# Kernel tuning notes

Hardware: AMD Instinct MI355X
Metric: run time of the kernel (lower is better)

## Reference

```python
import jax, jax.numpy as jnp
import numpy as np

BN_EPS = 1e-5

def conv1x1(x, w, b):
    # x: [B,C,H,W], w: [O,C], b: [O]
    return jnp.einsum('bchw,oc->bohw', x, w) + b[None, :, None, None]

def maxpool2x2(x):
    B, C, H, W = x.shape
    return x.reshape(B, C, H // 2, 2, W // 2, 2).max(axis=(3, 5))

def setup_inputs() -> dict:
    key = jax.random.key(0)
    ks = jax.random.split(key, 11)
    B, C, H, W = 8, 256, 64, 64
    Ci = C // 2  # inter_channels = 128
    s_in = 1.0 / np.sqrt(C)
    s_int = 1.0 / np.sqrt(Ci)
    return {
        'x': jax.random.normal(ks[0], (B, C, H, W), jnp.float32),
        'theta_w': jax.random.uniform(ks[1], (Ci, C), jnp.float32, -s_in, s_in),
        'theta_b': jax.random.uniform(ks[2], (Ci,), jnp.float32, -s_in, s_in),
        'phi_w': jax.random.uniform(ks[3], (Ci, C), jnp.float32, -s_in, s_in),
        'phi_b': jax.random.uniform(ks[4], (Ci,), jnp.float32, -s_in, s_in),
        'g_w': jax.random.uniform(ks[5], (Ci, C), jnp.float32, -s_in, s_in),
        'g_b': jax.random.uniform(ks[6], (Ci,), jnp.float32, -s_in, s_in),
        'W_w': jax.random.uniform(ks[7], (C, Ci), jnp.float32, -s_int, s_int),
        'W_b': jax.random.uniform(ks[8], (C,), jnp.float32, -s_int, s_int),
        'bn_gamma': jax.random.normal(ks[9], (C,), jnp.float32) * 0.1 + 1.0,
        'bn_beta': jax.random.normal(ks[10], (C,), jnp.float32) * 0.1,
    }

def reference(x, theta_w, theta_b, phi_w, phi_b, g_w, g_b, W_w, W_b, bn_gamma, bn_beta):
    B, C, H, W = x.shape
    Ci = theta_w.shape[0]
    # g and phi are sub-sampled (2x2 maxpool) after the 1x1 conv
    g_x = maxpool2x2(conv1x1(x, g_w, g_b)).reshape(B, Ci, -1)        # [B,Ci,M]
    g_x = g_x.transpose(0, 2, 1)                                     # [B,M,Ci]
    theta_x = conv1x1(x, theta_w, theta_b).reshape(B, Ci, -1)        # [B,Ci,N]
    theta_x = theta_x.transpose(0, 2, 1)                             # [B,N,Ci]
    phi_x = maxpool2x2(conv1x1(x, phi_w, phi_b)).reshape(B, Ci, -1)  # [B,Ci,M]
    f = jnp.einsum('bnc,bcm->bnm', theta_x, phi_x)                   # [B,N,M]
    f_div_C = jax.nn.softmax(f, axis=-1)
    y = jnp.einsum('bnm,bmc->bnc', f_div_C, g_x)                     # [B,N,Ci]
    y = y.transpose(0, 2, 1).reshape(B, Ci, H, W)
    # 1x1 conv + BatchNorm2d (training-mode batch statistics)
    W_y = conv1x1(y, W_w, W_b)
    mean = W_y.mean(axis=(0, 2, 3))
    var = W_y.var(axis=(0, 2, 3))
    W_y = (W_y - mean[None, :, None, None]) * jax.lax.rsqrt(var + BN_EPS)[None, :, None, None]
    W_y = W_y * bn_gamma[None, :, None, None] + bn_beta[None, :, None, None]
    return W_y + x
```

## Files before the change

### kernel.cpp

```cpp
#include <hip/hip_runtime.h>
#include <hip/hip_bf16.h>
#include <cstdint>
#include <math.h>

using bf16 = __hip_bfloat16;
typedef __attribute__((ext_vector_type(8))) short bf16x8;
typedef __attribute__((ext_vector_type(4))) float f32x4;

#define DEV __device__ __forceinline__

DEV float b2f(unsigned short u) { return __uint_as_float(((uint32_t)u) << 16); }
DEV float bfl(bf16 h) { return __bfloat162float(h); }
DEV short f2bs(float f) { bf16 h = __float2bfloat16(f); return *(short*)&h; }
DEV uint32_t pk2(float a, float b) {
  return (uint32_t)(unsigned short)f2bs(a) |
         ((uint32_t)(unsigned short)f2bs(b) << 16);
}
DEV float ldv(const void* p, int isbf, int i) {
  return isbf ? bfl(((const bf16*)p)[i]) : ((const float*)p)[i];
}

DEV bf16x8 load_wfrag(const void* w, int isbf, int row, int K, int off) {
  bf16x8 r;
  if (isbf) {
    r = *(const bf16x8*)((const short*)w + (size_t)row * K + off);
  } else {
    const float* f = (const float*)w + (size_t)row * K + off;
    float4 a = *(const float4*)f, b = *(const float4*)(f + 4);
    r[0] = f2bs(a.x); r[1] = f2bs(a.y); r[2] = f2bs(a.z); r[3] = f2bs(a.w);
    r[4] = f2bs(b.x); r[5] = f2bs(b.y); r[6] = f2bs(b.z); r[7] = f2bs(b.w);
  }
  return r;
}

__global__ __launch_bounds__(256) void sniff_kernel(
    const unsigned short* __restrict__ xr, int* __restrict__ flag)
{
  int tid = threadIdx.x;
  int good = 0;
  for (int k = tid; k < 16384; k += 256) {
    unsigned short u = xr[2 * k];
    int e = (u >> 7) & 0xFF;
    good += (e >= 0x6A && e <= 0x86) ? 1 : 0;
  }
  __shared__ int r[256];
  r[tid] = good;
  __syncthreads();
  for (int off = 128; off; off >>= 1) {
    if (tid < off) r[tid] += r[tid + off];
    __syncthreads();
  }
  if (tid == 0) *flag = (r[0] > 9830) ? 1 : 0;
}

__global__ __launch_bounds__(256) void transpose_x(
    const void* __restrict__ x, short* __restrict__ xT, const int* __restrict__ flag)
{
  const int isbf = *flag;
  __shared__ short lt[64 * 71];
  const int n0 = blockIdx.x * 64, c0 = blockIdx.y * 64, b = blockIdx.z;
  const int tid = threadIdx.x;
  for (int it = 0; it < 4; ++it) {
    int idx4 = it * 256 + tid;
    int ci = idx4 >> 4, n4 = (idx4 & 15) * 4;
    size_t go = ((size_t)(b * 256 + c0 + ci)) * 4096 + n0 + n4;
    if (isbf) {
      ushort4 v = *(const ushort4*)((const unsigned short*)x + go);
      lt[ci * 71 + n4 + 0] = v.x; lt[ci * 71 + n4 + 1] = v.y;
      lt[ci * 71 + n4 + 2] = v.z; lt[ci * 71 + n4 + 3] = v.w;
    } else {
      float4 v = *(const float4*)((const float*)x + go);
      lt[ci * 71 + n4 + 0] = f2bs(v.x); lt[ci * 71 + n4 + 1] = f2bs(v.y);
      lt[ci * 71 + n4 + 2] = f2bs(v.z); lt[ci * 71 + n4 + 3] = f2bs(v.w);
    }
  }
  __syncthreads();
  for (int it = 0; it < 4; ++it) {
    int idx4 = it * 256 + tid;
    int n = idx4 >> 4, c4 = (idx4 & 15) * 4;
    ushort4 v;
    v.x = (unsigned short)lt[(c4 + 0) * 71 + n];
    v.y = (unsigned short)lt[(c4 + 1) * 71 + n];
    v.z = (unsigned short)lt[(c4 + 2) * 71 + n];
    v.w = (unsigned short)lt[(c4 + 3) * 71 + n];
    *(ushort4*)(xT + ((size_t)(b * 4096 + n0 + n)) * 256 + c0 + c4) = v;
  }
}

__global__ __launch_bounds__(256) void conv_t_k(
    const short* __restrict__ xT, const void* __restrict__ w,
    const void* __restrict__ bias, short* __restrict__ out,
    const int* __restrict__ flag)
{
  const int isbf = *flag;
  __shared__ short sh[64 * 264];
  const int b = blockIdx.y, nbase = blockIdx.x * 64, tid = threadIdx.x;
  const int ln = tid & 15, q = (tid >> 4) & 3, wv = tid >> 6;
  for (int it = 0; it < 16; ++it) {
    int idx4 = it * 256 + tid;
    int n = idx4 >> 6, c4 = (idx4 & 63) * 4;
    *(ushort4*)&sh[n * 264 + c4] =
        *(const ushort4*)(xT + ((size_t)(b * 4096 + nbase + n)) * 256 + c4);
  }
  __syncthreads();
  f32x4 zero = {0.f, 0.f, 0.f, 0.f};
  f32x4 acc[4][2];
  for (int nt = 0; nt < 4; ++nt) for (int ti = 0; ti < 2; ++ti) acc[nt][ti] = zero;

  for (int kk = 0; kk < 8; ++kk) {
    int off = kk * 32 + q * 8;
    bf16x8 a[4];
    #pragma unroll
    for (int nt = 0; nt < 4; ++nt)
      a[nt] = *(const bf16x8*)&sh[(16 * nt + ln) * 264 + off];
    #pragma unroll
    for (int ti = 0; ti < 2; ++ti) {
      bf16x8 bw = load_wfrag(w, isbf, 16 * (2 * wv + ti) + ln, 256, off);
      #pragma unroll
      for (int nt = 0; nt < 4; ++nt)
        acc[nt][ti] = __builtin_amdgcn_mfma_f32_16x16x32_bf16(a[nt], bw, acc[nt][ti], 0, 0, 0);
    }
  }
  __syncthreads();
  float bv[2];
  for (int ti = 0; ti < 2; ++ti) bv[ti] = ldv(bias, isbf, 16 * (2 * wv + ti) + ln);
  for (int nt = 0; nt < 4; ++nt)
    for (int ti = 0; ti < 2; ++ti)
      for (int r = 0; r < 4; ++r)
        sh[(16 * nt + q * 4 + r) * 136 + 16 * (2 * wv + ti) + ln] =
            f2bs(acc[nt][ti][r] + bv[ti]);
  __syncthreads();
  for (int it = 0; it < 8; ++it) {
    int idx4 = it * 256 + tid;
    int n = idx4 >> 5, c4 = (idx4 & 31) * 4;
    *(ushort4*)(out + ((size_t)(b * 4096 + nbase + n)) * 128 + c4) =
        *(const ushort4*)&sh[n * 136 + c4];
  }
}

template<int CO, int K>
__global__ __launch_bounds__(256) void conv_n_k(
    const short* __restrict__ inp, const void* __restrict__ w,
    const void* __restrict__ bias, short* __restrict__ out,
    const int* __restrict__ flag)
{
  const int isbf = *flag;
  constexpr int XS = 64 * (K + 8);
  constexpr int OS = CO * 68;
  __shared__ short sh[(XS > OS ? XS : OS)];
  const int b = blockIdx.y, nbase = blockIdx.x * 64, tid = threadIdx.x;
  const int ln = tid & 15, q = (tid >> 4) & 3, wv = tid >> 6;
  constexpr int TPW = CO / 64;
  constexpr int KS = (K == 256) ? 6 : 5;
  for (int it = 0; it < 64 * K / 1024; ++it) {
    int idx4 = it * 256 + tid;
    int n = idx4 >> KS, c4 = (idx4 & ((K / 4) - 1)) * 4;
    *(ushort4*)&sh[n * (K + 8) + c4] =
        *(const ushort4*)(inp + ((size_t)(b * 4096 + nbase + n)) * K + c4);
  }
  __syncthreads();
  f32x4 zero = {0.f, 0.f, 0.f, 0.f};
  f32x4 acc[TPW][4];
  for (int ti = 0; ti < TPW; ++ti) for (int nt = 0; nt < 4; ++nt) acc[ti][nt] = zero;

  for (int kk = 0; kk < K / 32; ++kk) {
    int off = kk * 32 + q * 8;
    bf16x8 bx[4];
    #pragma unroll
    for (int nt = 0; nt < 4; ++nt)
      bx[nt] = *(const bf16x8*)&sh[(16 * nt + ln) * (K + 8) + off];
    #pragma unroll
    for (int ti = 0; ti < TPW; ++ti) {
      bf16x8 aw = load_wfrag(w, isbf, 16 * (TPW * wv + ti) + ln, K, off);
      #pragma unroll
      for (int nt = 0; nt < 4; ++nt)
        acc[ti][nt] = __builtin_amdgcn_mfma_f32_16x16x32_bf16(aw, bx[nt], acc[ti][nt], 0, 0, 0);
    }
  }
  __syncthreads();
  for (int ti = 0; ti < TPW; ++ti)
    for (int r = 0; r < 4; ++r) {
      int co = 16 * (TPW * wv + ti) + q * 4 + r;
      float bb = ldv(bias, isbf, co);
      for (int nt = 0; nt < 4; ++nt)
        sh[co * 68 + 16 * nt + ln] = f2bs(acc[ti][nt][r] + bb);
    }
  __syncthreads();
  for (int it = 0; it < 64 * CO / 1024; ++it) {
    int idx4 = it * 256 + tid;
    int co = idx4 >> 4, n4 = (idx4 & 15) * 4;
    *(ushort4*)(out + ((size_t)(b * CO + co)) * 4096 + nbase + n4) =
        *(const ushort4*)&sh[co * 68 + n4];
  }
}

__global__ __launch_bounds__(256) void pool_phi_kernel(
    const short* __restrict__ pc, short* __restrict__ phi)
{
  int idx = blockIdx.x * 256 + threadIdx.x;
  int ci = idx & 127, m = (idx >> 7) & 1023, b = idx >> 17;
  int mh = m >> 5, mw = m & 31;
  const short* p = pc + ((size_t)(b * 4096 + (mh * 2) * 64 + mw * 2)) * 128 + ci;
  float v = fmaxf(fmaxf(b2f(p[0]), b2f(p[128])),
                  fmaxf(b2f(p[64 * 128]), b2f(p[65 * 128])));
  phi[idx] = f2bs(v);
}

__global__ __launch_bounds__(256) void pool_g_kernel(
    const short* __restrict__ gc, short* __restrict__ g)
{
  int idx = blockIdx.x * 256 + threadIdx.x;
  int m = idx & 1023, bc = idx >> 10;
  int mh = m >> 5, mw = m & 31;
  const short* p = gc + (size_t)bc * 4096 + mh * 128 + mw * 2;
  float v = fmaxf(fmaxf(b2f(p[0]), b2f(p[1])), fmaxf(b2f(p[64]), b2f(p[65])));
  g[idx] = f2bs(v);
}

__global__ __launch_bounds__(256) void attn_kernel(
    const short* __restrict__ theta, const short* __restrict__ phi,
    const short* __restrict__ g, short* __restrict__ y)
{
  __shared__ short ph[64 * 136];
  __shared__ short gl[128 * 72];
  __shared__ short Pl[64 * 72];
  const int b = blockIdx.y, nbase = blockIdx.x * 64, tid = threadIdx.x;
  const int ln = tid & 15, q = (tid >> 4) & 3, wv = tid >> 6;

  const int pm  = tid >> 5;
  const int pc4 = (tid & 31) * 4;
  const int gci = tid >> 4;
  const int gm4 = (tid & 15) * 4;
  const short* phb = phi + (size_t)b * 1024 * 128;
  const short* gb  = g   + (size_t)b * 128 * 1024;

  ushort4 pf_p[8], pf_g[8];
  #pragma unroll
  for (int it = 0; it < 8; ++it)
    pf_p[it] = *(const ushort4*)(phb + ((size_t)(pm + 8 * it)) * 128 + pc4);
  #pragma unroll
  for (int it = 0; it < 8; ++it)
    pf_g[it] = *(const ushort4*)(gb + ((size_t)(gci + 16 * it)) * 1024 + gm4);

  bf16x8 a[4];
  #pragma unroll
  for (int kk = 0; kk < 4; ++kk)
    a[kk] = *(const bf16x8*)(theta +
        ((size_t)(b * 4096 + nbase + 16 * wv + ln)) * 128 + kk * 32 + q * 8);

  f32x4 zero = {0.f, 0.f, 0.f, 0.f};
  f32x4 yacc[8], lacc = zero;
  #pragma unroll
  for (int t = 0; t < 8; ++t) yacc[t] = zero;
  bf16x8 ones;
  #pragma unroll
  for (int j = 0; j < 8; ++j) ones[j] = 0x3F80;

  for (int mc = 0; mc < 16; ++mc) {
    #pragma unroll
    for (int it = 0; it < 8; ++it)
      *(ushort4*)&ph[(pm + 8 * it) * 136 + pc4] = pf_p[it];
    #pragma unroll
    for (int it = 0; it < 8; ++it)
      *(ushort4*)&gl[(gci + 16 * it) * 72 + gm4] = pf_g[it];
    __syncthreads();

    if (mc < 15) {
      const int nmc = mc + 1;
      #pragma unroll
      for (int it = 0; it < 8; ++it)
        pf_p[it] = *(const ushort4*)(phb +
            ((size_t)(nmc * 64 + pm + 8 * it)) * 128 + pc4);
      #pragma unroll
      for (int it = 0; it < 8; ++it)
        pf_g[it] = *(const ushort4*)(gb +
            ((size_t)(gci + 16 * it)) * 1024 + nmc * 64 + gm4);
    }

    #pragma unroll
    for (int t = 0; t < 4; ++t) {
      f32x4 s = zero;
      #pragma unroll
      for (int kk = 0; kk < 4; ++kk) {
        bf16x8 bp = *(const bf16x8*)&ph[(16 * t + ln) * 136 + kk * 32 + q * 8];
        s = __builtin_amdgcn_mfma_f32_16x16x32_bf16(a[kk], bp, s, 0, 0, 0);
      }
      #pragma unroll
      for (int r = 0; r < 4; ++r)
        Pl[(16 * wv + q * 4 + r) * 72 + 16 * t + ln] =
            f2bs(__expf(fminf(s[r], 80.f)));
    }
    bf16x8 ap[2];
    #pragma unroll
    for (int kk = 0; kk < 2; ++kk)
      ap[kk] = *(const bf16x8*)&Pl[(16 * wv + ln) * 72 + kk * 32 + q * 8];
    #pragma unroll
    for (int kk = 0; kk < 2; ++kk)
      lacc = __builtin_amdgcn_mfma_f32_16x16x32_bf16(ap[kk], ones, lacc, 0, 0, 0);
    #pragma unroll
    for (int t = 0; t < 8; ++t) {
      #pragma unroll
      for (int kk = 0; kk < 2; ++kk) {
        bf16x8 bg = *(const bf16x8*)&gl[(16 * t + ln) * 72 + kk * 32 + q * 8];
        yacc[t] = __builtin_amdgcn_mfma_f32_16x16x32_bf16(ap[kk], bg, yacc[t], 0, 0, 0);
      }
    }
    __syncthreads();
  }

  float li[4];
  #pragma unroll
  for (int r = 0; r < 4; ++r) li[r] = 1.0f / lacc[r];
  for (int t = 0; t < 8; ++t)
    for (int r = 0; r < 4; ++r)
      ph[(16 * wv + q * 4 + r) * 136 + 16 * t + ln] = f2bs(yacc[t][r] * li[r]);
  __syncthreads();
  for (int it = 0; it < 8; ++it) {
    int idx4 = it * 256 + tid;
    int n = idx4 >> 5, c4 = (idx4 & 31) * 4;
    *(ushort4*)(y + ((size_t)(b * 4096 + nbase + n)) * 128 + c4) =
        *(const ushort4*)&ph[n * 136 + c4];
  }
}

__global__ __launch_bounds__(256, 4) void convW_k(
    const short* __restrict__ yb, const void* __restrict__ w,
    const void* __restrict__ bias, short* __restrict__ Wy,
    float* __restrict__ stats, const int* __restrict__ flag)
{
  const int isbf = *flag;
  __shared__ short sh[256 * 72];
  const int b = blockIdx.y, nbase = blockIdx.x * 64, tid = threadIdx.x;
  const int ln = tid & 15, q = (tid >> 4) & 3, wv = tid >> 6;

  for (int it = 0; it < 4; ++it) {
    int idx8 = it * 256 + tid;
    int n = idx8 >> 4, c8 = (idx8 & 15) * 8;
    *(uint4*)&sh[n * 136 + c8] =
        *(const uint4*)(yb + ((size_t)(b * 4096 + nbase + n)) * 128 + c8);
  }
  __syncthreads();
  f32x4 zero = {0.f, 0.f, 0.f, 0.f};
  f32x4 acc[4][4];
  for (int ti = 0; ti < 4; ++ti)
    for (int nt = 0; nt < 4; ++nt) acc[ti][nt] = zero;

  for (int kk = 0; kk < 4; ++kk) {
    int off = kk * 32 + q * 8;
    bf16x8 bx[4];
    #pragma unroll
    for (int nt = 0; nt < 4; ++nt)
      bx[nt] = *(const bf16x8*)&sh[(16 * nt + ln) * 136 + off];
    #pragma unroll
    for (int ti = 0; ti < 4; ++ti) {
      bf16x8 aw = load_wfrag(w, isbf, 16 * (4 * wv + ti) + ln, 128, off);
      #pragma unroll
      for (int nt = 0; nt < 4; ++nt)
        acc[ti][nt] = __builtin_amdgcn_mfma_f32_16x16x32_bf16(aw, bx[nt], acc[ti][nt], 0, 0, 0);
    }
  }
  __syncthreads();
  #pragma unroll
  for (int ti = 0; ti < 4; ++ti)
    #pragma unroll
    for (int r = 0; r < 4; ++r) {
      int co = 16 * (4 * wv + ti) + 4 * q + r;
      float bb = ldv(bias, isbf, co);
      #pragma unroll
      for (int nt = 0; nt < 4; ++nt)
        sh[co * 72 + 16 * nt + ln] = f2bs(acc[ti][nt][r] + bb);
    }
  __syncthreads();
  {
    int co = tid;
    float s = 0.f, s2 = 0.f;
    for (int i = 0; i < 64; ++i) {
      float v = b2f((unsigned short)sh[co * 72 + i]);
      s += v; s2 += v * v;
    }
    atomicAdd(&stats[co], s);
    atomicAdd(&stats[256 + co], s2);
  }
  for (int it = 0; it < 8; ++it) {
    int idx8 = it * 256 + tid;
    int co = idx8 >> 3, n8 = (idx8 & 7) * 8;
    *(uint4*)(Wy + ((size_t)(b * 256 + co)) * 4096 + nbase + n8) =
        *(const uint4*)&sh[co * 72 + n8];
  }
}

__global__ __launch_bounds__(256) void bn_apply4(
    const short* __restrict__ Wy, const void* __restrict__ x,
    const float* __restrict__ stats, const void* __restrict__ gamma,
    const void* __restrict__ beta, void* __restrict__ out,
    const int* __restrict__ flag)
{
  const int isbf = *flag;
  int t = blockIdx.x * 256 + threadIdx.x;
  int idx4 = t * 4;
  int c = (idx4 >> 12) & 255;
  float s = stats[c], s2 = stats[256 + c];
  float mean = s * (1.0f / 32768.0f);
  float var = fmaxf(s2 * (1.0f / 32768.0f) - mean * mean, 0.f);
  float scale = rsqrtf(var + 1e-5f) * ldv(gamma, isbf, c);
  float shift = ldv(beta, isbf, c) - mean * scale;
  ushort4 wy = *(const ushort4*)(Wy + idx4);
  float xv[4];
  if (isbf) {
    ushort4 xu = *(const ushort4*)((const unsigned short*)x + idx4);
    xv[0] = b2f(xu.x); xv[1] = b2f(xu.y); xv[2] = b2f(xu.z); xv[3] = b2f(xu.w);
  } else {
    float4 xf = *(const float4*)((const float*)x + idx4);
    xv[0] = xf.x; xv[1] = xf.y; xv[2] = xf.z; xv[3] = xf.w;
  }
  float v0 = b2f(wy.x) * scale + shift + xv[0];
  float v1 = b2f(wy.y) * scale + shift + xv[1];
  float v2 = b2f(wy.z) * scale + shift + xv[2];
  float v3 = b2f(wy.w) * scale + shift + xv[3];
  if (isbf) {
    uint2 o; o.x = pk2(v0, v1); o.y = pk2(v2, v3);
    *(uint2*)((unsigned short*)out + idx4) = o;
  } else {
    float4 o = make_float4(v0, v1, v2, v3);
    *(float4*)((float*)out + idx4) = o;
  }
}

extern "C" void kernel_launch(void* const* d_in, const int* in_sizes, int n_in,
                              void* d_out, int out_size, void* d_ws, size_t ws_size,
                              hipStream_t stream) {
  const void* x       = d_in[0];
  const void* theta_w = d_in[1];
  const void* theta_b = d_in[2];
  const void* phi_w   = d_in[3];
  const void* phi_b   = d_in[4];
  const void* g_w     = d_in[5];
  const void* g_b     = d_in[6];
  const void* W_w     = d_in[7];
  const void* W_b     = d_in[8];
  const void* gamma   = d_in[9];
  const void* beta    = d_in[10];

  char* wsb = (char*)d_ws;
  short* xT      = (short*)(wsb + 0);
  short* ybuf    = (short*)(wsb + 0);
  short* theta   = (short*)(wsb + 16777216);
  short* W_y     = (short*)(wsb + 16777216);
  short* scratch = (short*)(wsb + 25165824);
  short* phi     = (short*)(wsb + 33554432);
  short* gg      = (short*)(wsb + 35651584);
  float* stats   = (float*)(wsb + 37748736);
  int*   flag    = (int*)  (wsb + 37750784);

  dim3 blk(256);
  dim3 cgrid(64, 8);
  dim3 tgrid(64, 4, 8);

  hipMemsetAsync(stats, 0, 2048, stream);
  sniff_kernel<<<1, blk, 0, stream>>>((const unsigned short*)x, flag);
  transpose_x<<<tgrid, blk, 0, stream>>>(x, xT, flag);
  conv_t_k<<<cgrid, blk, 0, stream>>>(xT, theta_w, theta_b, theta, flag);
  conv_t_k<<<cgrid, blk, 0, stream>>>(xT, phi_w, phi_b, scratch, flag);
  pool_phi_kernel<<<4096, blk, 0, stream>>>(scratch, phi);
  conv_n_k<128, 256><<<cgrid, blk, 0, stream>>>(xT, g_w, g_b, scratch, flag);
  pool_g_kernel<<<4096, blk, 0, stream>>>(scratch, gg);
  attn_kernel<<<cgrid, blk, 0, stream>>>(theta, phi, gg, ybuf);
  convW_k<<<cgrid, blk, 0, stream>>>(ybuf, W_w, W_b, W_y, stats, flag);
  bn_apply4<<<8192, blk, 0, stream>>>(W_y, x, stats, gamma, beta, d_out, flag);
}
```

Before: 246.7 us.

## Restructure attention kernel with 32x32 MFMA, register-resident P and split-M waves

The attention kernel now uses 32x32x16 bf16 MFMAs in a transposed formulation (phi as A, theta as B). The softmax probabilities are converted in registers with v_cvt_pk_bf16 and rearranged with v_permlane32_swap, so the LDS round trip for P goes away. Each wave handles a 32-row n-half and a 32-column m-half, and the partial y accumulators and row sums are combined through shared memory at the end. The shared-memory tiles use XOR swizzling with 16-byte loads, and the row-sum MFMA against a ones vector is replaced by scalar adds. The costs are more registers (launch bounds of 2), a cross-wave reduction epilogue, and reliance on gfx950-specific instructions.

Result: slower. 353.2 us (+43.2%).

```diff
diff --git a/kernel.cpp b/kernel.cpp
--- a/kernel.cpp
+++ b/kernel.cpp
@@ -6,6 +6,7 @@
 using bf16 = __hip_bfloat16;
 typedef __attribute__((ext_vector_type(8))) short bf16x8;
 typedef __attribute__((ext_vector_type(4))) float f32x4;
+typedef __attribute__((ext_vector_type(16))) float f32x16;
 
 #define DEV __device__ __forceinline__
 
@@ -18,6 +19,11 @@
 }
 DEV float ldv(const void* p, int isbf, int i) {
   return isbf ? bfl(((const bf16*)p)[i]) : ((const float*)p)[i];
+}
+DEV uint32_t cvtpk_bf16(float a, float b) {
+  uint32_t r;
+  asm("v_cvt_pk_bf16_f32 %0, %1, %2" : "=v"(r) : "v"(a), "v"(b));
+  return r;
 }
 
 DEV bf16x8 load_wfrag(const void* w, int isbf, int row, int K, int off) {
@@ -217,109 +223,152 @@
   g[idx] = f2bs(v);
 }
 
-__global__ __launch_bounds__(256) void attn_kernel(
+__global__ __launch_bounds__(256, 2) void attn_kernel(
     const short* __restrict__ theta, const short* __restrict__ phi,
     const short* __restrict__ g, short* __restrict__ y)
 {
-  __shared__ short ph[64 * 136];
-  __shared__ short gl[128 * 72];
-  __shared__ short Pl[64 * 72];
+  __shared__ alignas(16) char smem[51712];
+  char* phs = smem;
+  char* gls = smem + 16384;
+  float* comb = (float*)smem;
+  float* lred = (float*)(smem + 33792);
+  short* yout = (short*)(smem + 34304);
+
   const int b = blockIdx.y, nbase = blockIdx.x * 64, tid = threadIdx.x;
-  const int ln = tid & 15, q = (tid >> 4) & 3, wv = tid >> 6;
-
-  const int pm  = tid >> 5;
-  const int pc4 = (tid & 31) * 4;
-  const int gci = tid >> 4;
-  const int gm4 = (tid & 15) * 4;
+  const int l = tid & 63, wv = tid >> 6;
+  const int ln32 = l & 31, h = l >> 5;
+  const int nh = wv & 1, mh = wv >> 1;
+
   const short* phb = phi + (size_t)b * 1024 * 128;
   const short* gb  = g   + (size_t)b * 128 * 1024;
 
-  ushort4 pf_p[8], pf_g[8];
+  bf16x8 bth[8];
+  {
+    const short* tb = theta +
+        ((size_t)(b * 4096 + nbase + nh * 32 + ln32)) * 128 + h * 8;
+    #pragma unroll
+    for (int kk = 0; kk < 8; ++kk)
+      bth[kk] = *(const bf16x8*)(tb + kk * 16);
+  }
+
+  uint4 pf_p[4], pf_g[4];
   #pragma unroll
-  for (int it = 0; it < 8; ++it)
-    pf_p[it] = *(const ushort4*)(phb + ((size_t)(pm + 8 * it)) * 128 + pc4);
+  for (int it = 0; it < 4; ++it) {
+    int ch = it * 256 + tid;
+    int row = ch >> 4, sl = ch & 15;
+    pf_p[it] = *(const uint4*)(phb + ((size_t)row) * 128 + sl * 8);
+    int cr = ch >> 3, sg = ch & 7;
+    pf_g[it] = *(const uint4*)(gb + (size_t)cr * 1024 + sg * 8);
+  }
+
+  f32x16 yacc[4];
   #pragma unroll
-  for (int it = 0; it < 8; ++it)
-    pf_g[it] = *(const ushort4*)(gb + ((size_t)(gci + 16 * it)) * 1024 + gm4);
-
-  bf16x8 a[4];
+  for (int ct = 0; ct < 4; ++ct)
+    #pragma unroll
+    for (int r = 0; r < 16; ++r) yacc[ct][r] = 0.f;
+  float lsum = 0.f;
+
+  for (int mc = 0; mc < 16; ++mc) {
+    #pragma unroll
+    for (int it = 0; it < 4; ++it) {
+      int ch = it * 256 + tid;
+      int row = ch >> 4, sl = ch & 15;
+      *(uint4*)(phs + row * 256 + ((sl * 16) ^ ((row & 15) << 4))) = pf_p[it];
+    }
+    #pragma unroll
+    for (int it = 0; it < 4; ++it) {
+      int ch = it * 256 + tid;
+      int cr = ch >> 3, sg = ch & 7;
+      *(uint4*)(gls + cr * 128 + ((sg * 16) ^ ((cr & 7) << 4))) = pf_g[it];
+    }
+    __syncthreads();
+    if (mc < 15) {
+      int nm = mc + 1;
+      #pragma unroll
+      for (int it = 0; it < 4; ++it) {
+        int ch = it * 256 + tid;
+        int row = ch >> 4, sl = ch & 15;
+        pf_p[it] = *(const uint4*)(phb + ((size_t)(nm * 64 + row)) * 128 + sl * 8);
+        int cr = ch >> 3, sg = ch & 7;
+        pf_g[it] = *(const uint4*)(gb + (size_t)cr * 1024 + nm * 64 + sg * 8);
+      }
+    }
+
+    const int mrow = mh * 32 + ln32;
+    const char* pbase = phs + mrow * 256;
+    const int mxor = (mrow & 15) << 4;
+    f32x16 sA, sB;
+    #pragma unroll
+    for (int r = 0; r < 16; ++r) { sA[r] = 0.f; sB[r] = 0.f; }
+    #pragma unroll
+    for (int kk = 0; kk < 8; kk += 2) {
+      bf16x8 a0 = *(const bf16x8*)(pbase + ((kk * 32 + h * 16) ^ mxor));
+      bf16x8 a1 = *(const bf16x8*)(pbase + (((kk + 1) * 32 + h * 16) ^ mxor));
+      sA = __builtin_amdgcn_mfma_f32_32x32x16_bf16(a0, bth[kk], sA, 0, 0, 0);
+      sB = __builtin_amdgcn_mfma_f32_32x32x16_bf16(a1, bth[kk + 1], sB, 0, 0, 0);
+    }
+    float p[16];
+    #pragma unroll
+    for (int r = 0; r < 16; ++r) {
+      p[r] = __expf(fminf(sA[r] + sB[r], 80.f));
+      lsum += p[r];
+    }
+    uint32_t cc[8];
+    #pragma unroll
+    for (int r = 0; r < 8; ++r) cc[r] = cvtpk_bf16(p[2 * r], p[2 * r + 1]);
+    asm volatile("v_permlane32_swap_b32 %0, %1" : "+v"(cc[0]), "+v"(cc[2]));
+    asm volatile("v_permlane32_swap_b32 %0, %1" : "+v"(cc[1]), "+v"(cc[3]));
+    asm volatile("v_permlane32_swap_b32 %0, %1" : "+v"(cc[4]), "+v"(cc[6]));
+    asm volatile("v_permlane32_swap_b32 %0, %1" : "+v"(cc[5]), "+v"(cc[7]));
+    bf16x8 pa0 = *(const bf16x8*)&cc[0];
+    bf16x8 pa1 = *(const bf16x8*)&cc[4];
+
+    #pragma unroll
+    for (int ct = 0; ct < 4; ++ct) {
+      const char* gbase = gls + (ct * 32 + ln32) * 128;
+      const int gxor = (ln32 & 7) << 4;
+      bf16x8 g0 = *(const bf16x8*)(gbase + ((mh * 64 + h * 16) ^ gxor));
+      bf16x8 g1 = *(const bf16x8*)(gbase + ((mh * 64 + 32 + h * 16) ^ gxor));
+      yacc[ct] = __builtin_amdgcn_mfma_f32_32x32x16_bf16(pa0, g0, yacc[ct], 0, 0, 0);
+      yacc[ct] = __builtin_amdgcn_mfma_f32_32x32x16_bf16(pa1, g1, yacc[ct], 0, 0, 0);
+    }
+    __syncthreads();
+  }
+
+  float lf = lsum + __shfl_xor(lsum, 32);
   #pragma unroll
-  for (int kk = 0; kk < 4; ++kk)
-    a[kk] = *(const bf16x8*)(theta +
-        ((size_t)(b * 4096 + nbase + 16 * wv + ln)) * 128 + kk * 32 + q * 8);
-
-  f32x4 zero = {0.f, 0.f, 0.f, 0.f};
-  f32x4 yacc[8], lacc = zero;
+  for (int tt = 0; tt < 2; ++tt) {
+    int ct = (1 - mh) * 2 + tt;
+    #pragma unroll
+    for (int r = 0; r < 16; ++r) {
+      int n = (r & 3) + 8 * (r >> 2) + 4 * h;
+      comb[((nh * 4 + ct) * 32 + ln32) * 33 + n] = yacc[ct][r];
+    }
+  }
+  if (l < 32) lred[mh * 64 + nh * 32 + l] = lf;
+  __syncthreads();
+  float linv[16];
   #pragma unroll
-  for (int t = 0; t < 8; ++t) yacc[t] = zero;
-  bf16x8 ones;
+  for (int r = 0; r < 16; ++r) {
+    int n = (r & 3) + 8 * (r >> 2) + 4 * h;
+    linv[r] = 1.0f / (lred[nh * 32 + n] + lred[64 + nh * 32 + n]);
+  }
   #pragma unroll
-  for (int j = 0; j < 8; ++j) ones[j] = 0x3F80;
-
-  for (int mc = 0; mc < 16; ++mc) {
-    #pragma unroll
-    for (int it = 0; it < 8; ++it)
-      *(ushort4*)&ph[(pm + 8 * it) * 136 + pc4] = pf_p[it];
-    #pragma unroll
-    for (int it = 0; it < 8; ++it)
-      *(ushort4*)&gl[(gci + 16 * it) * 72 + gm4] = pf_g[it];
-    __syncthreads();
-
-    if (mc < 15) {
-      const int nmc = mc + 1;
-      #pragma unroll
-      for (int it = 0; it < 8; ++it)
-        pf_p[it] = *(const ushort4*)(phb +
-            ((size_t)(nmc * 64 + pm + 8 * it)) * 128 + pc4);
-      #pragma unroll
-      for (int it = 0; it < 8; ++it)
-        pf_g[it] = *(const ushort4*)(gb +
-            ((size_t)(gci + 16 * it)) * 1024 + nmc * 64 + gm4);
-    }
-
-    #pragma unroll
-    for (int t = 0; t < 4; ++t) {
-      f32x4 s = zero;
-      #pragma unroll
-      for (int kk = 0; kk < 4; ++kk) {
-        bf16x8 bp = *(const bf16x8*)&ph[(16 * t + ln) * 136 + kk * 32 + q * 8];
-        s = __builtin_amdgcn_mfma_f32_16x16x32_bf16(a[kk], bp, s, 0, 0, 0);
-      }
-      #pragma unroll
-      for (int r = 0; r < 4; ++r)
-        Pl[(16 * wv + q * 4 + r) * 72 + 16 * t + ln] =
-            f2bs(__expf(fminf(s[r], 80.f)));
-    }
-    bf16x8 ap[2];
-    #pragma unroll
-    for (int kk = 0; kk < 2; ++kk)
-      ap[kk] = *(const bf16x8*)&Pl[(16 * wv + ln) * 72 + kk * 32 + q * 8];
-    #pragma unroll
-    for (int kk = 0; kk < 2; ++kk)
-      lacc = __builtin_amdgcn_mfma_f32_16x16x32_bf16(ap[kk], ones, lacc, 0, 0, 0);
-    #pragma unroll
-    for (int t = 0; t < 8; ++t) {
-      #pragma unroll
-      for (int kk = 0; kk < 2; ++kk) {
-        bf16x8 bg = *(const bf16x8*)&gl[(16 * t + ln) * 72 + kk * 32 + q * 8];
-        yacc[t] = __builtin_amdgcn_mfma_f32_16x16x32_bf16(ap[kk], bg, yacc[t], 0, 0, 0);
-      }
-    }
-    __syncthreads();
-  }
-
-  float li[4];
-  #pragma unroll
-  for (int r = 0; r < 4; ++r) li[r] = 1.0f / lacc[r];
-  for (int t = 0; t < 8; ++t)
-    for (int r = 0; r < 4; ++r)
-      ph[(16 * wv + q * 4 + r) * 136 + 16 * t + ln] = f2bs(yacc[t][r] * li[r]);
+  for (int tt = 0; tt < 2; ++tt) {
+    int ct = mh * 2 + tt;
+    #pragma unroll
+    for (int r = 0; r < 16; ++r) {
+      int n = (r & 3) + 8 * (r >> 2) + 4 * h;
+      float v = yacc[ct][r] + comb[((nh * 4 + ct) * 32 + ln32) * 33 + n];
+      yout[(nh * 32 + n) * 136 + ct * 32 + ln32] = f2bs(v * linv[r]);
+    }
+  }
   __syncthreads();
   for (int it = 0; it < 8; ++it) {
     int idx4 = it * 256 + tid;
     int n = idx4 >> 5, c4 = (idx4 & 31) * 4;
     *(ushort4*)(y + ((size_t)(b * 4096 + nbase + n)) * 128 + c4) =
-        *(const ushort4*)&ph[n * 136 + c4];
+        *(const ushort4*)&yout[n * 136 + c4];
   }
 }
 
```
